# Optimization experiments

Hardware: AMD Instinct MI355X
Metric: run time of the kernel (lower is better)

## Reference

```python
import jax, jax.numpy as jnp
import numpy as np

PHASE_BINS = 100
EPS = 1e-10
W_AMP = 0.5
W_PHASE = 0.5


def setup_inputs() -> dict:
    key = jax.random.key(0)
    kA, kB = jax.random.split(key)
    A = jax.random.normal(kA, (64, 2, 512, 512), dtype=jnp.float32)
    B = jax.random.normal(kB, (64, 2, 512, 512), dtype=jnp.float32)
    return {"A": A, "B": B}


def _to_complex(x):
    # (batch, 2, H, W) -> complex (batch, H, W)
    return jax.lax.complex(x[:, 0, :, :], x[:, 1, :, :])


def _kl(p, q):
    # torch.sum over the last TWO dims (faithful: for 2D [batch,bins] phase
    # histograms this collapses to a scalar, like the original code).
    return jnp.sum(p * jnp.log((p + EPS) / (q + EPS)), axis=(-2, -1))


def _phase_hist_density(phase, edges):
    # phase: (batch, H, W). torch.histogram with density=True.
    b = phase.shape[0]
    n = phase.shape[1] * phase.shape[2]
    flat = phase.reshape(b, n)
    # rightmost edge inclusive in last bin (torch semantics)
    idx = jnp.clip(jnp.searchsorted(edges, flat, side="right") - 1, 0, PHASE_BINS - 1)
    counts = jax.vmap(
        lambda i: jnp.zeros((PHASE_BINS,), jnp.float32).at[i].add(1.0)
    )(idx)
    width = edges[1:] - edges[:-1]  # (bins,)
    return counts / (jnp.float32(n) * width)  # density


def reference(A, B):
    edges = jnp.linspace(-np.pi, np.pi, PHASE_BINS + 1, dtype=jnp.float32)
    Ac = _to_complex(A)
    Bc = _to_complex(B)

    # amplitude KL, shape (batch,)
    Aa = jnp.abs(Ac)
    Ba = jnp.abs(Bc)
    P = Aa / (jnp.sum(Aa, axis=(-2, -1), keepdims=True) + EPS)
    Q = Ba / (jnp.sum(Ba, axis=(-2, -1), keepdims=True) + EPS)
    amp_loss = _kl(P, Q)

    # phase KL (scalar, summed over batch per original dim=(-2,-1) on 2D hist)
    Pp = _phase_hist_density(jnp.angle(Ac), edges)
    Qp = _phase_hist_density(jnp.angle(Bc), edges)
    Pp = Pp / (jnp.sum(Pp, axis=-1, keepdims=True) + EPS)
    Qp = Qp / (jnp.sum(Qp, axis=-1, keepdims=True) + EPS)
    phase_loss = _kl(Pp, Qp)

    return W_AMP * amp_loss + W_PHASE * phase_loss
```

## Files before the change

kernel.cpp:

```cpp
#include <hip/hip_runtime.h>
#include <math.h>

#define PHASE_BINS 100
#define EPSF 1e-10f
#define HW 262144
#define BATCH 64
#define BLOCKS_PER_BATCH 32
#define CHUNK (HW / BLOCKS_PER_BATCH)
#define THREADS 256

__device__ __forceinline__ float wave_reduce_sum(float v) {
    #pragma unroll
    for (int off = 32; off > 0; off >>= 1) v += __shfl_down(v, off, 64);
    return v;
}

__global__ __launch_bounds__(THREADS) void pass1_kernel(
    const float* __restrict__ A, const float* __restrict__ B,
    float* __restrict__ SA, float* __restrict__ SB, float* __restrict__ Tacc,
    unsigned int* __restrict__ histA, unsigned int* __restrict__ histB)
{
    __shared__ unsigned int h[2][4][PHASE_BINS];
    const int wave = threadIdx.x >> 6;
    const int lane = threadIdx.x & 63;

    for (int i = threadIdx.x; i < 2 * 4 * PHASE_BINS; i += THREADS)
        ((unsigned int*)h)[i] = 0u;
    __syncthreads();

    const int b   = blockIdx.x / BLOCKS_PER_BATCH;
    const int blk = blockIdx.x % BLOCKS_PER_BATCH;
    const size_t base = (size_t)b * (2 * HW);
    const float* Ar = A + base;
    const float* Ai = Ar + HW;
    const float* Br = B + base;
    const float* Bi = Br + HW;
    const int start = blk * CHUNK;

    const float PI_F = 3.14159265358979323846f;
    const float inv_step = (float)PHASE_BINS / (2.0f * PI_F);

    float sA = 0.f, sB = 0.f, t = 0.f;

    for (int i = threadIdx.x * 4; i < CHUNK; i += THREADS * 4) {
        const int idx = start + i;
        float4 ar4 = *(const float4*)(Ar + idx);
        float4 ai4 = *(const float4*)(Ai + idx);
        float4 br4 = *(const float4*)(Br + idx);
        float4 bi4 = *(const float4*)(Bi + idx);
        const float* arp = (const float*)&ar4;
        const float* aip = (const float*)&ai4;
        const float* brp = (const float*)&br4;
        const float* bip = (const float*)&bi4;
        #pragma unroll
        for (int j = 0; j < 4; ++j) {
            float arj = arp[j], aij = aip[j];
            float brj = brp[j], bij = bip[j];
            float aa = sqrtf(arj * arj + aij * aij);
            float bb = sqrtf(brj * brj + bij * bij);
            sA += aa;
            sB += bb;
            if (aa > 0.f)
                t += aa * (__logf(aa) - __logf(fmaxf(bb, 1e-37f)));
            float pa = atan2f(aij, arj);
            float pb = atan2f(bij, brj);
            int ka = (int)floorf((pa + PI_F) * inv_step);
            int kb = (int)floorf((pb + PI_F) * inv_step);
            ka = min(max(ka, 0), PHASE_BINS - 1);
            kb = min(max(kb, 0), PHASE_BINS - 1);
            atomicAdd(&h[0][wave][ka], 1u);
            atomicAdd(&h[1][wave][kb], 1u);
        }
    }

    sA = wave_reduce_sum(sA);
    sB = wave_reduce_sum(sB);
    t  = wave_reduce_sum(t);
    if (lane == 0) {
        atomicAdd(&SA[b], sA);
        atomicAdd(&SB[b], sB);
        atomicAdd(&Tacc[b], t);
    }

    __syncthreads();
    if (threadIdx.x < PHASE_BINS) {
        int bin = threadIdx.x;
        unsigned v = h[0][0][bin] + h[0][1][bin] + h[0][2][bin] + h[0][3][bin];
        atomicAdd(&histA[b * PHASE_BINS + bin], v);
    } else if (threadIdx.x < 2 * PHASE_BINS) {
        int bin = threadIdx.x - PHASE_BINS;
        unsigned v = h[1][0][bin] + h[1][1][bin] + h[1][2][bin] + h[1][3][bin];
        atomicAdd(&histB[b * PHASE_BINS + bin], v);
    }
}

__global__ __launch_bounds__(256) void pass2_kernel(
    const float* __restrict__ SA, const float* __restrict__ SB,
    const float* __restrict__ T,
    const unsigned int* __restrict__ histA, const unsigned int* __restrict__ histB,
    float* __restrict__ out)
{
    __shared__ float amp_sh[BATCH];
    __shared__ float wave_phase[4];
    const int wave = threadIdx.x >> 6;
    const int lane = threadIdx.x & 63;
    const float PI_F = 3.14159265358979323846f;
    const float step = (2.0f * PI_F) / PHASE_BINS;

    float local_phase = 0.f;
    for (int b = wave; b < BATCH; b += 4) {
        float d_a[2], d_b[2];
        float sum_a = 0.f, sum_b = 0.f;
        #pragma unroll
        for (int r = 0; r < 2; ++r) {
            int bin = lane + r * 64;
            float da = 0.f, db = 0.f;
            if (bin < PHASE_BINS) {
                float e0 = -PI_F + bin * step;
                float e1 = (bin == PHASE_BINS - 1) ? PI_F : (-PI_F + (bin + 1) * step);
                float w = e1 - e0;
                float denom = (float)HW * w;
                da = (float)histA[b * PHASE_BINS + bin] / denom;
                db = (float)histB[b * PHASE_BINS + bin] / denom;
            }
            d_a[r] = da; d_b[r] = db;
            sum_a += da; sum_b += db;
        }
        #pragma unroll
        for (int off = 32; off > 0; off >>= 1) {
            sum_a += __shfl_xor(sum_a, off, 64);
            sum_b += __shfl_xor(sum_b, off, 64);
        }
        float kl = 0.f;
        #pragma unroll
        for (int r = 0; r < 2; ++r) {
            int bin = lane + r * 64;
            if (bin < PHASE_BINS) {
                float p = d_a[r] / (sum_a + EPSF);
                float q = d_b[r] / (sum_b + EPSF);
                kl += p * logf((p + EPSF) / (q + EPSF));
            }
        }
        #pragma unroll
        for (int off = 32; off > 0; off >>= 1) kl += __shfl_xor(kl, off, 64);
        if (lane == 0) {
            local_phase += kl;
            float sa_raw = SA[b];
            float sa = sa_raw + EPSF;
            float sb = SB[b] + EPSF;
            amp_sh[b] = T[b] / sa + (sa_raw / sa) * logf(sb / sa);
        }
    }
    if (lane == 0) wave_phase[wave] = local_phase;
    __syncthreads();
    float phase_total = wave_phase[0] + wave_phase[1] + wave_phase[2] + wave_phase[3];
    if (threadIdx.x < BATCH)
        out[threadIdx.x] = 0.5f * amp_sh[threadIdx.x] + 0.5f * phase_total;
}

extern "C" void kernel_launch(void* const* d_in, const int* in_sizes, int n_in,
                              void* d_out, int out_size, void* d_ws, size_t ws_size,
                              hipStream_t stream) {
    const float* A = (const float*)d_in[0];
    const float* B = (const float*)d_in[1];
    float* out = (float*)d_out;

    float* SA = (float*)d_ws;
    float* SB = SA + BATCH;
    float* T  = SB + BATCH;
    unsigned int* histA = (unsigned int*)(T + BATCH);
    unsigned int* histB = histA + BATCH * PHASE_BINS;

    size_t zero_bytes = (size_t)(3 * BATCH) * sizeof(float)
                      + (size_t)(2 * BATCH * PHASE_BINS) * sizeof(unsigned int);
    hipMemsetAsync(d_ws, 0, zero_bytes, stream);

    pass1_kernel<<<dim3(BATCH * BLOCKS_PER_BATCH), dim3(THREADS), 0, stream>>>(
        A, B, SA, SB, T, histA, histB);
    pass2_kernel<<<1, 256, 0, stream>>>(SA, SB, T, histA, histB, out);
}
```

Baseline: 331.9 us.

## Use fast atan2 binning, single-log KL, lane-split histograms, more blocks

Replaces atan2f plus floor with a polynomial atan approximation that maps straight to a phase bin. It computes the amplitude KL term with a single log2 of the squared-magnitude ratio and uses hardware sqrt and rcp intrinsics. Each wave's shared histogram is split into two copies by lane parity to reduce LDS atomic contention, and blocks per batch double from 32 to 64. The approximate atan and rcp can move values that sit near bin edges into a neighbouring bin, and the clamped ratio slightly changes the handling of zero magnitudes.

```diff
diff --git a/kernel.cpp b/kernel.cpp
--- a/kernel.cpp
+++ b/kernel.cpp
@@ -5,8 +5,8 @@
 #define EPSF 1e-10f
 #define HW 262144
 #define BATCH 64
-#define BLOCKS_PER_BATCH 32
-#define CHUNK (HW / BLOCKS_PER_BATCH)
+#define BPB 64
+#define CHUNK (HW / BPB)
 #define THREADS 256
 
 __device__ __forceinline__ float wave_reduce_sum(float v) {
@@ -15,30 +15,50 @@
     return v;
 }
 
+__device__ __forceinline__ int phase_bin(float y, float x) {
+    const float PI_F = 3.14159265358979323846f;
+    float ax = fabsf(x), ay = fabsf(y);
+    float mx = fmaxf(ax, ay), mn = fminf(ax, ay);
+    float r  = mn * __builtin_amdgcn_rcpf(mx);
+    float rr = (r - 1.0f) * __builtin_amdgcn_rcpf(r + 1.0f);
+    bool big = r > 0.4142135624f;
+    float z = big ? rr : r;
+    float s = z * z;
+    float p = fmaf(fmaf(fmaf(8.05374449538e-2f, s, -1.38776856032e-1f), s,
+                        1.99777106478e-1f), s, -3.33329491539e-1f);
+    float th = fmaf(z * s, p, z);
+    th += big ? 0.78539816340f : 0.0f;
+    th = (ay > ax) ? 1.57079632679f - th : th;
+    th = (x < 0.0f) ? PI_F - th : th;
+    th = (y < 0.0f) ? -th : th;
+    int bin = (int)((th + PI_F) * 15.9154943092f);
+    return min(max(bin, 0), PHASE_BINS - 1);
+}
+
 __global__ __launch_bounds__(THREADS) void pass1_kernel(
     const float* __restrict__ A, const float* __restrict__ B,
     float* __restrict__ SA, float* __restrict__ SB, float* __restrict__ Tacc,
     unsigned int* __restrict__ histA, unsigned int* __restrict__ histB)
 {
-    __shared__ unsigned int h[2][4][PHASE_BINS];
+    __shared__ unsigned int h[2][4][2][PHASE_BINS];
     const int wave = threadIdx.x >> 6;
     const int lane = threadIdx.x & 63;
 
-    for (int i = threadIdx.x; i < 2 * 4 * PHASE_BINS; i += THREADS)
+    for (int i = threadIdx.x; i < 2 * 4 * 2 * PHASE_BINS; i += THREADS)
         ((unsigned int*)h)[i] = 0u;
     __syncthreads();
 
-    const int b   = blockIdx.x / BLOCKS_PER_BATCH;
-    const int blk = blockIdx.x % BLOCKS_PER_BATCH;
+    unsigned int* __restrict__ hA = &h[0][wave][lane & 1][0];
+    unsigned int* __restrict__ hB = &h[1][wave][lane & 1][0];
+
+    const int b   = blockIdx.x / BPB;
+    const int blk = blockIdx.x % BPB;
     const size_t base = (size_t)b * (2 * HW);
     const float* Ar = A + base;
     const float* Ai = Ar + HW;
     const float* Br = B + base;
     const float* Bi = Br + HW;
     const int start = blk * CHUNK;
-
-    const float PI_F = 3.14159265358979323846f;
-    const float inv_step = (float)PHASE_BINS / (2.0f * PI_F);
 
     float sA = 0.f, sB = 0.f, t = 0.f;
 
@@ -56,20 +76,17 @@
         for (int j = 0; j < 4; ++j) {
             float arj = arp[j], aij = aip[j];
             float brj = brp[j], bij = bip[j];
-            float aa = sqrtf(arj * arj + aij * aij);
-            float bb = sqrtf(brj * brj + bij * bij);
+            float ra2 = fmaf(arj, arj, aij * aij);
+            float rb2 = fmaf(brj, brj, bij * bij);
+            float aa = __builtin_amdgcn_sqrtf(ra2);
+            float bb = __builtin_amdgcn_sqrtf(rb2);
             sA += aa;
             sB += bb;
-            if (aa > 0.f)
-                t += aa * (__logf(aa) - __logf(fmaxf(bb, 1e-37f)));
-            float pa = atan2f(aij, arj);
-            float pb = atan2f(bij, brj);
-            int ka = (int)floorf((pa + PI_F) * inv_step);
-            int kb = (int)floorf((pb + PI_F) * inv_step);
-            ka = min(max(ka, 0), PHASE_BINS - 1);
-            kb = min(max(kb, 0), PHASE_BINS - 1);
-            atomicAdd(&h[0][wave][ka], 1u);
-            atomicAdd(&h[1][wave][kb], 1u);
+            float q = ra2 * __builtin_amdgcn_rcpf(rb2);
+            q = fminf(fmaxf(q, 1e-37f), 1e37f);
+            t = fmaf(aa * 0.34657359028f, __log2f(q), t);
+            atomicAdd(hA + phase_bin(aij, arj), 1u);
+            atomicAdd(hB + phase_bin(bij, brj), 1u);
         }
     }
 
@@ -83,14 +100,15 @@
     }
 
     __syncthreads();
-    if (threadIdx.x < PHASE_BINS) {
-        int bin = threadIdx.x;
-        unsigned v = h[0][0][bin] + h[0][1][bin] + h[0][2][bin] + h[0][3][bin];
-        atomicAdd(&histA[b * PHASE_BINS + bin], v);
-    } else if (threadIdx.x < 2 * PHASE_BINS) {
-        int bin = threadIdx.x - PHASE_BINS;
-        unsigned v = h[1][0][bin] + h[1][1][bin] + h[1][2][bin] + h[1][3][bin];
-        atomicAdd(&histB[b * PHASE_BINS + bin], v);
+    if (threadIdx.x < 2 * PHASE_BINS) {
+        int hi  = threadIdx.x / PHASE_BINS;
+        int bin = threadIdx.x % PHASE_BINS;
+        unsigned v = 0;
+        #pragma unroll
+        for (int w = 0; w < 4; ++w)
+            v += h[hi][w][0][bin] + h[hi][w][1][bin];
+        unsigned int* dst = hi ? histB : histA;
+        atomicAdd(&dst[b * PHASE_BINS + bin], v);
     }
 }
 
@@ -175,7 +193,7 @@
                       + (size_t)(2 * BATCH * PHASE_BINS) * sizeof(unsigned int);
     hipMemsetAsync(d_ws, 0, zero_bytes, stream);
 
-    pass1_kernel<<<dim3(BATCH * BLOCKS_PER_BATCH), dim3(THREADS), 0, stream>>>(
+    pass1_kernel<<<dim3(BATCH * BPB), dim3(THREADS), 0, stream>>>(
         A, B, SA, SB, T, histA, histB);
     pass2_kernel<<<1, 256, 0, stream>>>(SA, SB, T, histA, histB, out);
 }
```

Result: slower. 360.1 us (+8.5%).
